# Kernel optimization log

Hardware: AMD Instinct MI355X
Metric: run time of the kernel (lower is better)

The kernel has to match this reference:

```python
import jax, jax.numpy as jnp
import numpy as np

# SamplesLoss(loss='sinkhorn', p=1, blur=0.05): entropic regularization eps = blur**p = 0.05,
# debiased Sinkhorn divergence S(a,b) = OT(a,b) - 0.5*OT(a,a) - 0.5*OT(b,b).
EPS = 0.05
N_ITER = 50
N_POINTS = 32


def _cost(X, Y):
    # p=1 cost: Euclidean distance. X:[B,N,D] Y:[B,M,D] -> [B,N,M]
    d2 = jnp.sum((X[:, :, None, :] - Y[:, None, :, :]) ** 2, axis=-1)
    return jnp.sqrt(d2 + 1e-12)


def _ot(X, Y):
    # log-domain Sinkhorn with uniform weights; returns dual cost <mu,f>+<nu,g> per batch.
    B, N, _ = X.shape
    M = Y.shape[1]
    C = _cost(X, Y)  # [B,N,M]
    log_mu = jnp.full((B, N), -np.log(N), C.dtype)
    log_nu = jnp.full((B, M), -np.log(M), C.dtype)

    def body(carry, _):
        f, g = carry
        f = -EPS * jax.nn.logsumexp((g[:, None, :] - C) / EPS + log_nu[:, None, :], axis=2)
        g = -EPS * jax.nn.logsumexp((f[:, :, None] - C) / EPS + log_mu[:, :, None], axis=1)
        return (f, g), None

    init = (jnp.zeros((B, N), C.dtype), jnp.zeros((B, M), C.dtype))
    (f, g), _ = jax.lax.scan(body, init, None, length=N_ITER)
    return jnp.mean(f, axis=-1) + jnp.mean(g, axis=-1)  # uniform weights => mean


def _sinkhorn_div(X, Y):
    return _ot(X, Y) - 0.5 * _ot(X, X) - 0.5 * _ot(Y, Y)


def _encode(x, W, edge_index):
    # simple 1-layer GCN-style encoder: linear + mean neighbor aggregation + self, ReLU
    h = x @ W  # [n_nodes, emb_dim]
    src, dst = edge_index[0], edge_index[1]
    n = x.shape[0]
    agg = jax.ops.segment_sum(h[src], dst, num_segments=n)
    deg = jax.ops.segment_sum(jnp.ones(src.shape, h.dtype), dst, num_segments=n)
    return jax.nn.relu(h + agg / jnp.maximum(deg, 1.0)[:, None])


def setup_inputs() -> dict:
    key = jax.random.key(0)
    k1, k2, k3, k4, k5 = jax.random.split(key, 5)
    n_nodes, d_feat, emb_dim = 50000, 128, 256
    n_edges, n_pairs = 800000, 8192
    x = jax.random.normal(k1, (n_nodes, d_feat), jnp.float32)
    W = jax.random.normal(k2, (d_feat, emb_dim), jnp.float32) / np.sqrt(d_feat)
    edge_index = jax.random.randint(k3, (2, n_edges), 0, n_nodes, jnp.int64)
    pairs = jax.random.randint(k4, (2, n_pairs), 0, n_nodes, jnp.int64)
    graph_dist = jax.random.uniform(k5, (n_pairs,), jnp.float32, 1.0, 5.0)
    return {"x": x, "W": W, "edge_index": edge_index, "pairs": pairs,
            "graph_dist": graph_dist}


def reference(x, W, edge_index, pairs, graph_dist):
    z = _encode(x, W, edge_index)                       # [n_nodes, emb_dim]
    B = pairs.shape[1]
    Xa = z[pairs[0]].reshape(B, N_POINTS, -1)           # [B, n_points, space_dim]
    Xb = z[pairs[1]].reshape(B, N_POINTS, -1)
    distance = _sinkhorn_div(Xa, Xb)                    # = -score_pairs
    distortion = jnp.abs(distance - graph_dist) / graph_dist
    return jnp.mean(distortion)
```

## Files before the change

kernel.cpp:

```cpp
#include <hip/hip_runtime.h>

#define N_NODES 50000
#define N_EDGES 800000
#define N_PAIRS 8192
#define N_SLOTS (2 * N_PAIRS)
#define CAP     64

#define INV_EPS   20.0f
#define LOG2E_F   1.4426950408889634f
#define LN2_F     0.6931471805599453f
#define LN32_F    3.4657359027997265f
#define EPS_F     0.05f

typedef float f2 __attribute__((ext_vector_type(2)));

__global__ void k_mark(const int* __restrict__ pairs, int* __restrict__ flags) {
    int t = blockIdx.x * 256 + threadIdx.x;
    if (t < N_SLOTS) flags[pairs[t]] = 1;
}

__global__ __launch_bounds__(256) void k_scatter(
        const int* __restrict__ eidx, const int* __restrict__ flags,
        int* __restrict__ cnt, int* __restrict__ bucket) {
    int t = blockIdx.x * 256 + threadIdx.x;
    int dst = eidx[N_EDGES + t];
    if (!flags[dst]) return;
    int pos = atomicAdd(&cnt[dst], 1);
    if (pos < CAP) bucket[dst * CAP + pos] = eidx[t];
}

__global__ __launch_bounds__(256) void k_gemm(
        const int* __restrict__ pairs, const float* __restrict__ x,
        const int* __restrict__ cnt, const int* __restrict__ bucket,
        const float* __restrict__ W, float* __restrict__ Z) {
    __shared__ __align__(16) float Us[16 * 128];
    int sbase = blockIdx.x * 16;
    int t = threadIdx.x;
    int wave = t >> 6, lane = t & 63;

    #pragma unroll
    for (int rr = 0; rr < 4; ++rr) {
        int r = wave * 4 + rr;
        int node = pairs[sbase + r];
        int n = cnt[node];
        int m = (n < CAP) ? n : CAP;
        const int* bk = bucket + node * CAP;
        float ax = 0.0f, ay = 0.0f;
        int k = 0;
        for (; k + 4 <= m; k += 4) {
            int s0 = bk[k], s1 = bk[k + 1], s2 = bk[k + 2], s3 = bk[k + 3];
            float2 v0 = *(const float2*)(x + (size_t)s0 * 128 + lane * 2);
            float2 v1 = *(const float2*)(x + (size_t)s1 * 128 + lane * 2);
            float2 v2 = *(const float2*)(x + (size_t)s2 * 128 + lane * 2);
            float2 v3 = *(const float2*)(x + (size_t)s3 * 128 + lane * 2);
            ax += (v0.x + v1.x) + (v2.x + v3.x);
            ay += (v0.y + v1.y) + (v2.y + v3.y);
        }
        for (; k < m; ++k) {
            int s0 = bk[k];
            float2 v0 = *(const float2*)(x + (size_t)s0 * 128 + lane * 2);
            ax += v0.x;
            ay += v0.y;
        }
        float rdeg = 1.0f / fmaxf((float)n, 1.0f);
        float2 xv = *(const float2*)(x + (size_t)node * 128 + lane * 2);
        float2 o;
        o.x = fmaf(ax, rdeg, xv.x);
        o.y = fmaf(ay, rdeg, xv.y);
        *(float2*)(Us + r * 128 + lane * 2) = o;
    }
    __syncthreads();

    int jq = t & 63;
    int rq = t >> 6;
    float acc[4][4] = {};
    const float4* Wv = (const float4*)W;

    for (int k4 = 0; k4 < 32; ++k4) {
        float4 wv[4];
        #pragma unroll
        for (int i = 0; i < 4; ++i) wv[i] = Wv[(size_t)(k4 * 4 + i) * 64 + jq];
        #pragma unroll
        for (int r = 0; r < 4; ++r) {
            float4 uv = *(const float4*)(Us + (rq * 4 + r) * 128 + k4 * 4);
            float uk0 = uv.x, uk1 = uv.y, uk2 = uv.z, uk3 = uv.w;
            acc[r][0] = fmaf(uk0, wv[0].x, acc[r][0]);
            acc[r][1] = fmaf(uk0, wv[0].y, acc[r][1]);
            acc[r][2] = fmaf(uk0, wv[0].z, acc[r][2]);
            acc[r][3] = fmaf(uk0, wv[0].w, acc[r][3]);
            acc[r][0] = fmaf(uk1, wv[1].x, acc[r][0]);
            acc[r][1] = fmaf(uk1, wv[1].y, acc[r][1]);
            acc[r][2] = fmaf(uk1, wv[1].z, acc[r][2]);
            acc[r][3] = fmaf(uk1, wv[1].w, acc[r][3]);
            acc[r][0] = fmaf(uk2, wv[2].x, acc[r][0]);
            acc[r][1] = fmaf(uk2, wv[2].y, acc[r][1]);
            acc[r][2] = fmaf(uk2, wv[2].z, acc[r][2]);
            acc[r][3] = fmaf(uk2, wv[2].w, acc[r][3]);
            acc[r][0] = fmaf(uk3, wv[3].x, acc[r][0]);
            acc[r][1] = fmaf(uk3, wv[3].y, acc[r][1]);
            acc[r][2] = fmaf(uk3, wv[3].z, acc[r][2]);
            acc[r][3] = fmaf(uk3, wv[3].w, acc[r][3]);
        }
    }

    #pragma unroll
    for (int r = 0; r < 4; ++r) {
        float4 o;
        o.x = fmaxf(acc[r][0], 0.0f);
        o.y = fmaxf(acc[r][1], 0.0f);
        o.z = fmaxf(acc[r][2], 0.0f);
        o.w = fmaxf(acc[r][3], 0.0f);
        *(float4*)(Z + (size_t)(sbase + rq * 4 + r) * 256 + jq * 4) = o;
    }
}

__global__ __launch_bounds__(128) void k_sinkhorn(
        const float* __restrict__ Z, float* __restrict__ dist) {
    __shared__ __align__(16) float smem[2][640];

    int w = threadIdx.x >> 6;
    int lane = threadIdx.x & 63;
    const float CSCALE = -INV_EPS * LOG2E_F;
    const float CBIAS  = -LN32_F * LOG2E_F;

    if (blockIdx.x >= 4096) {
        float* sX = &smem[w][0];
        float* sY = &smem[w][256];
        float* sf = &smem[w][512];
        float* sg = &smem[w][544];
        float* su = &smem[w][576];
        float* sv = &smem[w][608];

        int b = (blockIdx.x - 4096) * 2 + w;
        int sx = b, sy = N_PAIRS + b;

        *(float4*)(&sX[lane * 4]) = ((const float4*)(Z + (size_t)sx * 256))[lane];
        *(float4*)(&sY[lane * 4]) = ((const float4*)(Z + (size_t)sy * 256))[lane];
        sg[lane & 31] = 0.0f;

        int i_r = lane & 31, jh = lane >> 5;
        int j_c = lane & 31, ih = lane >> 5;

        f2 CrowV[8], CcolV[8];
        {
            const f2* xp = (const f2*)(&sX[i_r * 8]);
            f2 x0 = xp[0], x1 = xp[1], x2 = xp[2], x3 = xp[3];
            #pragma unroll
            for (int t = 0; t < 16; ++t) {
                int j = jh * 16 + t;
                const f2* yp = (const f2*)(&sY[j * 8]);
                f2 d, s2;
                d = x0 - yp[0]; s2 = d * d;
                d = x1 - yp[1]; s2 = __builtin_elementwise_fma(d, d, s2);
                d = x2 - yp[2]; s2 = __builtin_elementwise_fma(d, d, s2);
                d = x3 - yp[3]; s2 = __builtin_elementwise_fma(d, d, s2);
                float d2 = s2.x + s2.y + 1e-12f;
                CrowV[t >> 1][t & 1] = fmaf(__builtin_amdgcn_sqrtf(d2), CSCALE, CBIAS);
            }
            const f2* yp = (const f2*)(&sY[j_c * 8]);
            f2 y0 = yp[0], y1 = yp[1], y2 = yp[2], y3 = yp[3];
            #pragma unroll
            for (int t = 0; t < 16; ++t) {
                int i = ih * 16 + t;
                const f2* qp = (const f2*)(&sX[i * 8]);
                f2 d, s2;
                d = qp[0] - y0; s2 = d * d;
                d = qp[1] - y1; s2 = __builtin_elementwise_fma(d, d, s2);
                d = qp[2] - y2; s2 = __builtin_elementwise_fma(d, d, s2);
                d = qp[3] - y3; s2 = __builtin_elementwise_fma(d, d, s2);
                float d2 = s2.x + s2.y + 1e-12f;
                CcolV[t >> 1][t & 1] = fmaf(__builtin_amdgcn_sqrtf(d2), CSCALE, CBIAS);
            }
        }

        float ft = 0.0f, gt = 0.0f;

        #pragma unroll 1
        for (int it = 0; it < 2; ++it) {
            {
                const float4* gp = (const float4*)(&sg[jh * 16]);
                float4 G0 = gp[0], G1 = gp[1], G2 = gp[2], G3 = gp[3];
                f2 gv[8] = {f2{G0.x, G0.y}, f2{G0.z, G0.w}, f2{G1.x, G1.y}, f2{G1.z, G1.w},
                            f2{G2.x, G2.y}, f2{G2.z, G2.w}, f2{G3.x, G3.y}, f2{G3.z, G3.w}};
                f2 val[8], m2 = f2{-1e30f, -1e30f};
                #pragma unroll
                for (int t2 = 0; t2 < 8; ++t2) {
                    val[t2] = gv[t2] + CrowV[t2];
                    m2 = __builtin_elementwise_max(m2, val[t2]);
                }
                float m = fmaxf(m2.x, m2.y);
                m = fmaxf(m, __shfl_xor(m, 32));
                f2 mm = f2{m, m};
                float s0 = 0.0f, s1 = 0.0f;
                #pragma unroll
                for (int t2 = 0; t2 < 8; ++t2) {
                    f2 e = val[t2] - mm;
                    s0 += __builtin_amdgcn_exp2f(e.x);
                    s1 += __builtin_amdgcn_exp2f(e.y);
                }
                float s = s0 + s1;
                s += __shfl_xor(s, 32);
                ft = -(m + __builtin_amdgcn_logf(s));
            }
            sf[lane & 31] = ft;
            {
                const float4* fp = (const float4*)(&sf[ih * 16]);
                float4 F0 = fp[0], F1 = fp[1], F2 = fp[2], F3 = fp[3];
                f2 fv[8] = {f2{F0.x, F0.y}, f2{F0.z, F0.w}, f2{F1.x, F1.y}, f2{F1.z, F1.w},
                            f2{F2.x, F2.y}, f2{F2.z, F2.w}, f2{F3.x, F3.y}, f2{F3.z, F3.w}};
                f2 val[8], m2 = f2{-1e30f, -1e30f};
                #pragma unroll
                for (int t2 = 0; t2 < 8; ++t2) {
                    val[t2] = fv[t2] + CcolV[t2];
                    m2 = __builtin_elementwise_max(m2, val[t2]);
                }
                float m = fmaxf(m2.x, m2.y);
                m = fmaxf(m, __shfl_xor(m, 32));
                f2 mm = f2{m, m};
                float s0 = 0.0f, s1 = 0.0f;
                #pragma unroll
                for (int t2 = 0; t2 < 8; ++t2) {
                    f2 e = val[t2] - mm;
                    s0 += __builtin_amdgcn_exp2f(e.x);
                    s1 += __builtin_amdgcn_exp2f(e.y);
                }
                float s = s0 + s1;
                s += __shfl_xor(s, 32);
                gt = -(m + __builtin_amdgcn_logf(s));
            }
            sg[lane & 31] = gt;
        }

        f2 KR2[8], KC2[8];
        float ureg = 1.0f, vreg = 1.0f;

        auto absorb = [&]() {
            const float4* gp = (const float4*)(&sg[jh * 16]);
            float4 G0 = gp[0], G1 = gp[1], G2 = gp[2], G3 = gp[3];
            f2 gv[8] = {f2{G0.x, G0.y}, f2{G0.z, G0.w}, f2{G1.x, G1.y}, f2{G1.z, G1.w},
                        f2{G2.x, G2.y}, f2{G2.z, G2.w}, f2{G3.x, G3.y}, f2{G3.z, G3.w}};
            f2 ftv = f2{ft, ft};
            #pragma unroll
            for (int t2 = 0; t2 < 8; ++t2) {
                f2 a = (gv[t2] + CrowV[t2]) + ftv;
                KR2[t2].x = __builtin_amdgcn_exp2f(a.x);
                KR2[t2].y = __builtin_amdgcn_exp2f(a.y);
            }
            const float4* fp = (const float4*)(&sf[ih * 16]);
            float4 F0 = fp[0], F1 = fp[1], F2 = fp[2], F3 = fp[3];
            f2 fv[8] = {f2{F0.x, F0.y}, f2{F0.z, F0.w}, f2{F1.x, F1.y}, f2{F1.z, F1.w},
                        f2{F2.x, F2.y}, f2{F2.z, F2.w}, f2{F3.x, F3.y}, f2{F3.z, F3.w}};
            f2 gtv = f2{gt, gt};
            #pragma unroll
            for (int t2 = 0; t2 < 8; ++t2) {
                f2 a = (fv[t2] + CcolV[t2]) + gtv;
                KC2[t2].x = __builtin_amdgcn_exp2f(a.x);
                KC2[t2].y = __builtin_amdgcn_exp2f(a.y);
            }
            sv[lane & 31] = 1.0f;
            ureg = 1.0f;
            vreg = 1.0f;
        };

        const int blens[5] = {6, 6, 12, 12, 12};
        absorb();
        #pragma unroll 1
        for (int blk = 0; blk < 5; ++blk) {
            int L = blens[blk];
            #pragma unroll 2
            for (int s6 = 0; s6 < L; ++s6) {
                {
                    const float4* vp = (const float4*)(&sv[jh * 16]);
                    float4 A0 = vp[0], A1 = vp[1], A2 = vp[2], A3 = vp[3];
                    f2 acc0 = KR2[0] * f2{A0.x, A0.y};
                    f2 acc1 = KR2[1] * f2{A0.z, A0.w};
                    acc0 = __builtin_elementwise_fma(KR2[2], f2{A1.x, A1.y}, acc0);
                    acc1 = __builtin_elementwise_fma(KR2[3], f2{A1.z, A1.w}, acc1);
                    acc0 = __builtin_elementwise_fma(KR2[4], f2{A2.x, A2.y}, acc0);
                    acc1 = __builtin_elementwise_fma(KR2[5], f2{A2.z, A2.w}, acc1);
                    acc0 = __builtin_elementwise_fma(KR2[6], f2{A3.x, A3.y}, acc0);
                    acc1 = __builtin_elementwise_fma(KR2[7], f2{A3.z, A3.w}, acc1);
                    f2 a = acc0 + acc1;
                    float S = a.x + a.y;
                    S += __shfl_xor(S, 32);
                    ureg = __builtin_amdgcn_rcpf(S);
                }
                su[lane & 31] = ureg;
                {
                    const float4* up = (const float4*)(&su[ih * 16]);
                    float4 A0 = up[0], A1 = up[1], A2 = up[2], A3 = up[3];
                    f2 acc0 = KC2[0] * f2{A0.x, A0.y};
                    f2 acc1 = KC2[1] * f2{A0.z, A0.w};
                    acc0 = __builtin_elementwise_fma(KC2[2], f2{A1.x, A1.y}, acc0);
                    acc1 = __builtin_elementwise_fma(KC2[3], f2{A1.z, A1.w}, acc1);
                    acc0 = __builtin_elementwise_fma(KC2[4], f2{A2.x, A2.y}, acc0);
                    acc1 = __builtin_elementwise_fma(KC2[5], f2{A2.z, A2.w}, acc1);
                    acc0 = __builtin_elementwise_fma(KC2[6], f2{A3.x, A3.y}, acc0);
                    acc1 = __builtin_elementwise_fma(KC2[7], f2{A3.z, A3.w}, acc1);
                    f2 a = acc0 + acc1;
                    float T = a.x + a.y;
                    T += __shfl_xor(T, 32);
                    vreg = __builtin_amdgcn_rcpf(T);
                }
                sv[lane & 31] = vreg;
            }
            if (blk < 4) {
                ft += __builtin_amdgcn_logf(ureg);
                gt += __builtin_amdgcn_logf(vreg);
                sf[lane & 31] = ft;
                sg[lane & 31] = gt;
                absorb();
            }
        }
        ft += __builtin_amdgcn_logf(ureg);
        gt += __builtin_amdgcn_logf(vreg);

        float v = ft + gt;
        #pragma unroll
        for (int off = 32; off > 0; off >>= 1) v += __shfl_xor(v, off);
        if (lane == 0) {
            float cost = v * (EPS_F * LN2_F / 64.0f);
            unsafeAtomicAdd(&dist[b], cost);
        }
    } else {
        int h = lane >> 5, i = lane & 31;
        int q = (i >> 4) & 1;
        int ip = i ^ 16;
        int P = blockIdx.x * 2 + w;
        int src = h ? (N_PAIRS + P) : P;

        float* sP  = &smem[w][h * 256];
        float* swv = &smem[w][512];
        float* spv = &smem[w][576];

        {
            const float4* zp = (const float4*)(Z + (size_t)src * 256);
            *(float4*)(&sP[i * 8])     = zp[i * 2];
            *(float4*)(&sP[i * 8 + 4]) = zp[i * 2 + 1];
        }

        f2 CA[8], CB[8];
        {
            const f2* xp = (const f2*)(&sP[i * 8]);
            f2 x0 = xp[0], x1 = xp[1], x2 = xp[2], x3 = xp[3];
            const f2* bp = (const f2*)(&sP[ip * 8]);
            f2 b0 = bp[0], b1 = bp[1], b2 = bp[2], b3 = bp[3];
            #pragma unroll
            for (int t = 0; t < 16; ++t) {
                int j = q * 16 + t;
                const f2* yp = (const f2*)(&sP[j * 8]);
                f2 y0 = yp[0], y1 = yp[1], y2 = yp[2], y3 = yp[3];
                f2 d, s2;
                d = x0 - y0; s2 = d * d;
                d = x1 - y1; s2 = __builtin_elementwise_fma(d, d, s2);
                d = x2 - y2; s2 = __builtin_elementwise_fma(d, d, s2);
                d = x3 - y3; s2 = __builtin_elementwise_fma(d, d, s2);
                float d2 = s2.x + s2.y + 1e-12f;
                CA[t >> 1][t & 1] = fmaf(__builtin_amdgcn_sqrtf(d2), CSCALE, CBIAS);
                d = b0 - y0; s2 = d * d;
                d = b1 - y1; s2 = __builtin_elementwise_fma(d, d, s2);
                d = b2 - y2; s2 = __builtin_elementwise_fma(d, d, s2);
                d = b3 - y3; s2 = __builtin_elementwise_fma(d, d, s2);
                float e2 = s2.x + s2.y + 1e-12f;
                CB[t >> 1][t & 1] = fmaf(__builtin_amdgcn_sqrtf(e2), CSCALE, CBIAS);
            }
        }

        float pp = 0.0f, E = 1.0f, wcur = 1.0f, wprev = 1.0f;
        f2 KA[8], KB[8];
        #pragma unroll
        for (int t = 0; t < 8; ++t) {
            KA[t].x = __builtin_amdgcn_exp2f(CA[t].x);
            KA[t].y = __builtin_amdgcn_exp2f(CA[t].y);
            KB[t].x = __builtin_amdgcn_exp2f(CB[t].x);
            KB[t].y = __builtin_amdgcn_exp2f(CB[t].y);
        }
        swv[lane] = 1.0f;

        const int blens[9] = {4, 12, 12, 12, 12, 12, 12, 12, 12};
        #pragma unroll 1
        for (int blk = 0; blk < 9; ++blk) {
            int L = blens[blk];
            #pragma unroll 2
            for (int s = 0; s < L; ++s) {
                const float4* wp = (const float4*)(&swv[h * 32 + q * 16]);
                float4 A0 = wp[0], A1 = wp[1], A2 = wp[2], A3 = wp[3];
                f2 aA0 = KA[0] * f2{A0.x, A0.y};
                f2 aA1 = KA[1] * f2{A0.z, A0.w};
                f2 aB0 = KB[0] * f2{A0.x, A0.y};
                f2 aB1 = KB[1] * f2{A0.z, A0.w};
                aA0 = __builtin_elementwise_fma(KA[2], f2{A1.x, A1.y}, aA0);
                aA1 = __builtin_elementwise_fma(KA[3], f2{A1.z, A1.w}, aA1);
                aB0 = __builtin_elementwise_fma(KB[2], f2{A1.x, A1.y}, aB0);
                aB1 = __builtin_elementwise_fma(KB[3], f2{A1.z, A1.w}, aB1);
                aA0 = __builtin_elementwise_fma(KA[4], f2{A2.x, A2.y}, aA0);
                aA1 = __builtin_elementwise_fma(KA[5], f2{A2.z, A2.w}, aA1);
                aB0 = __builtin_elementwise_fma(KB[4], f2{A2.x, A2.y}, aB0);
                aB1 = __builtin_elementwise_fma(KB[5], f2{A2.z, A2.w}, aB1);
                aA0 = __builtin_elementwise_fma(KA[6], f2{A3.x, A3.y}, aA0);
                aA1 = __builtin_elementwise_fma(KA[7], f2{A3.z, A3.w}, aA1);
                aB0 = __builtin_elementwise_fma(KB[6], f2{A3.x, A3.y}, aB0);
                aB1 = __builtin_elementwise_fma(KB[7], f2{A3.z, A3.w}, aB1);
                f2 aa = aA0 + aA1;
                f2 bb = aB0 + aB1;
                float pa = aa.x + aa.y;
                float pb = bb.x + bb.y;
                float other = __shfl_xor(pb, 16);
                float S = pa + other;
                wprev = wcur;
                wcur = __builtin_amdgcn_rcpf(S) * E;
                swv[h * 32 + i] = wcur;
            }
            if (blk < 8) {
                pp += __builtin_amdgcn_logf(wcur);
                spv[lane] = pp;
                const float4* pv = (const float4*)(&spv[h * 32 + q * 16]);
                float4 P0 = pv[0], P1 = pv[1], P2 = pv[2], P3 = pv[3];
                f2 pj[8] = {f2{P0.x,P0.y}, f2{P0.z,P0.w}, f2{P1.x,P1.y}, f2{P1.z,P1.w},
                            f2{P2.x,P2.y}, f2{P2.z,P2.w}, f2{P3.x,P3.y}, f2{P3.z,P3.w}};
                #pragma unroll
                for (int t = 0; t < 8; ++t) {
                    f2 a = pj[t] + CA[t];
                    KA[t].x = __builtin_amdgcn_exp2f(a.x);
                    KA[t].y = __builtin_amdgcn_exp2f(a.y);
                    f2 c = pj[t] + CB[t];
                    KB[t].x = __builtin_amdgcn_exp2f(c.x);
                    KB[t].y = __builtin_amdgcn_exp2f(c.y);
                }
                E = __builtin_amdgcn_exp2f(-pp);
                wcur = 1.0f;
                swv[lane] = 1.0f;
            }
        }

        float zsum = 2.0f * pp + __builtin_amdgcn_logf(wprev)
                   + __builtin_amdgcn_logf(wcur);
        #pragma unroll
        for (int off = 16; off > 0; off >>= 1) zsum += __shfl_xor(zsum, off);
        if (i == 0) {
            float cost = zsum * (EPS_F * LN2_F / 32.0f);
            unsafeAtomicAdd(&dist[P], -0.5f * cost);
        }
    }
}

__global__ void k_finalize(const float* __restrict__ dist,
                           const float* __restrict__ gd, float* __restrict__ out) {
    __shared__ float red[256];
    float s = 0.0f;
    for (int i = threadIdx.x; i < N_PAIRS; i += 256) {
        float g = gd[i];
        s += fabsf(dist[i] - g) / g;
    }
    red[threadIdx.x] = s;
    __syncthreads();
    for (int o = 128; o > 0; o >>= 1) {
        if (threadIdx.x < o) red[threadIdx.x] += red[threadIdx.x + o];
        __syncthreads();
    }
    if (threadIdx.x == 0) out[0] = red[0] * (1.0f / N_PAIRS);
}

extern "C" void kernel_launch(void* const* d_in, const int* in_sizes, int n_in,
                              void* d_out, int out_size, void* d_ws, size_t ws_size,
                              hipStream_t stream) {
    const float* x    = (const float*)d_in[0];
    const float* W    = (const float*)d_in[1];
    const int*   eidx = (const int*)d_in[2];
    const int*   pair = (const int*)d_in[3];
    const float* gd   = (const float*)d_in[4];

    char* ws = (char*)d_ws;
    size_t off = 0;
    int*   cnt    = (int*)  (ws + off); off += (size_t)N_NODES * 4;
    int*   flags  = (int*)  (ws + off); off += (size_t)N_NODES * 4;
    float* dist   = (float*)(ws + off); off += (size_t)N_PAIRS * 4;
    size_t zero_bytes = off;
    int*   bucket = (int*)  (ws + off); off += (size_t)N_NODES * CAP * 4;
    float* Z      = (float*)(ws + off); off += (size_t)N_SLOTS * 256 * 4;

    hipMemsetAsync(d_ws, 0, zero_bytes, stream);
    k_mark    <<<(N_SLOTS + 255) / 256, 256, 0, stream>>>(pair, flags);
    k_scatter <<<N_EDGES / 256, 256, 0, stream>>>(eidx, flags, cnt, bucket);
    k_gemm    <<<N_SLOTS / 16, 256, 0, stream>>>(pair, x, cnt, bucket, W, Z);
    k_sinkhorn<<<8192, 128, 0, stream>>>(Z, dist);
    k_finalize<<<1, 256, 0, stream>>>(dist, gd, (float*)d_out);
}
```

Baseline: 252.0 us.

## Process one cross-pair per half-wave and update Sinkhorn kernels multiplicatively

The cross OT(X,Y) path now gives each 32-lane half-wave a whole problem, one row per lane, instead of splitting rows across two halves that needed cross-half shuffles. This halves the blocks needed for the cross pairs, so the launch shrinks from 8192 to 6144 blocks. Both paths now refresh the Gibbs kernel at each absorption by multiplying the existing entries by exp of the dual increments, rather than recomputing exp from the full potentials. Registers per lane roughly double (32-entry cost rows and columns), which may lower occupancy, and the multiplicative update may accumulate rounding drift.

```diff
diff --git a/kernel.cpp b/kernel.cpp
--- a/kernel.cpp
+++ b/kernel.cpp
@@ -116,222 +116,24 @@
 
 __global__ __launch_bounds__(128) void k_sinkhorn(
         const float* __restrict__ Z, float* __restrict__ dist) {
-    __shared__ __align__(16) float smem[2][640];
+    __shared__ __align__(16) float smem[2][1280];
 
     int w = threadIdx.x >> 6;
     int lane = threadIdx.x & 63;
+    float* S = &smem[w][0];
     const float CSCALE = -INV_EPS * LOG2E_F;
     const float CBIAS  = -LN32_F * LOG2E_F;
 
-    if (blockIdx.x >= 4096) {
-        float* sX = &smem[w][0];
-        float* sY = &smem[w][256];
-        float* sf = &smem[w][512];
-        float* sg = &smem[w][544];
-        float* su = &smem[w][576];
-        float* sv = &smem[w][608];
-
-        int b = (blockIdx.x - 4096) * 2 + w;
-        int sx = b, sy = N_PAIRS + b;
-
-        *(float4*)(&sX[lane * 4]) = ((const float4*)(Z + (size_t)sx * 256))[lane];
-        *(float4*)(&sY[lane * 4]) = ((const float4*)(Z + (size_t)sy * 256))[lane];
-        sg[lane & 31] = 0.0f;
-
-        int i_r = lane & 31, jh = lane >> 5;
-        int j_c = lane & 31, ih = lane >> 5;
-
-        f2 CrowV[8], CcolV[8];
-        {
-            const f2* xp = (const f2*)(&sX[i_r * 8]);
-            f2 x0 = xp[0], x1 = xp[1], x2 = xp[2], x3 = xp[3];
-            #pragma unroll
-            for (int t = 0; t < 16; ++t) {
-                int j = jh * 16 + t;
-                const f2* yp = (const f2*)(&sY[j * 8]);
-                f2 d, s2;
-                d = x0 - yp[0]; s2 = d * d;
-                d = x1 - yp[1]; s2 = __builtin_elementwise_fma(d, d, s2);
-                d = x2 - yp[2]; s2 = __builtin_elementwise_fma(d, d, s2);
-                d = x3 - yp[3]; s2 = __builtin_elementwise_fma(d, d, s2);
-                float d2 = s2.x + s2.y + 1e-12f;
-                CrowV[t >> 1][t & 1] = fmaf(__builtin_amdgcn_sqrtf(d2), CSCALE, CBIAS);
-            }
-            const f2* yp = (const f2*)(&sY[j_c * 8]);
-            f2 y0 = yp[0], y1 = yp[1], y2 = yp[2], y3 = yp[3];
-            #pragma unroll
-            for (int t = 0; t < 16; ++t) {
-                int i = ih * 16 + t;
-                const f2* qp = (const f2*)(&sX[i * 8]);
-                f2 d, s2;
-                d = qp[0] - y0; s2 = d * d;
-                d = qp[1] - y1; s2 = __builtin_elementwise_fma(d, d, s2);
-                d = qp[2] - y2; s2 = __builtin_elementwise_fma(d, d, s2);
-                d = qp[3] - y3; s2 = __builtin_elementwise_fma(d, d, s2);
-                float d2 = s2.x + s2.y + 1e-12f;
-                CcolV[t >> 1][t & 1] = fmaf(__builtin_amdgcn_sqrtf(d2), CSCALE, CBIAS);
-            }
-        }
-
-        float ft = 0.0f, gt = 0.0f;
-
-        #pragma unroll 1
-        for (int it = 0; it < 2; ++it) {
-            {
-                const float4* gp = (const float4*)(&sg[jh * 16]);
-                float4 G0 = gp[0], G1 = gp[1], G2 = gp[2], G3 = gp[3];
-                f2 gv[8] = {f2{G0.x, G0.y}, f2{G0.z, G0.w}, f2{G1.x, G1.y}, f2{G1.z, G1.w},
-                            f2{G2.x, G2.y}, f2{G2.z, G2.w}, f2{G3.x, G3.y}, f2{G3.z, G3.w}};
-                f2 val[8], m2 = f2{-1e30f, -1e30f};
-                #pragma unroll
-                for (int t2 = 0; t2 < 8; ++t2) {
-                    val[t2] = gv[t2] + CrowV[t2];
-                    m2 = __builtin_elementwise_max(m2, val[t2]);
-                }
-                float m = fmaxf(m2.x, m2.y);
-                m = fmaxf(m, __shfl_xor(m, 32));
-                f2 mm = f2{m, m};
-                float s0 = 0.0f, s1 = 0.0f;
-                #pragma unroll
-                for (int t2 = 0; t2 < 8; ++t2) {
-                    f2 e = val[t2] - mm;
-                    s0 += __builtin_amdgcn_exp2f(e.x);
-                    s1 += __builtin_amdgcn_exp2f(e.y);
-                }
-                float s = s0 + s1;
-                s += __shfl_xor(s, 32);
-                ft = -(m + __builtin_amdgcn_logf(s));
-            }
-            sf[lane & 31] = ft;
-            {
-                const float4* fp = (const float4*)(&sf[ih * 16]);
-                float4 F0 = fp[0], F1 = fp[1], F2 = fp[2], F3 = fp[3];
-                f2 fv[8] = {f2{F0.x, F0.y}, f2{F0.z, F0.w}, f2{F1.x, F1.y}, f2{F1.z, F1.w},
-                            f2{F2.x, F2.y}, f2{F2.z, F2.w}, f2{F3.x, F3.y}, f2{F3.z, F3.w}};
-                f2 val[8], m2 = f2{-1e30f, -1e30f};
-                #pragma unroll
-                for (int t2 = 0; t2 < 8; ++t2) {
-                    val[t2] = fv[t2] + CcolV[t2];
-                    m2 = __builtin_elementwise_max(m2, val[t2]);
-                }
-                float m = fmaxf(m2.x, m2.y);
-                m = fmaxf(m, __shfl_xor(m, 32));
-                f2 mm = f2{m, m};
-                float s0 = 0.0f, s1 = 0.0f;
-                #pragma unroll
-                for (int t2 = 0; t2 < 8; ++t2) {
-                    f2 e = val[t2] - mm;
-                    s0 += __builtin_amdgcn_exp2f(e.x);
-                    s1 += __builtin_amdgcn_exp2f(e.y);
-                }
-                float s = s0 + s1;
-                s += __shfl_xor(s, 32);
-                gt = -(m + __builtin_amdgcn_logf(s));
-            }
-            sg[lane & 31] = gt;
-        }
-
-        f2 KR2[8], KC2[8];
-        float ureg = 1.0f, vreg = 1.0f;
-
-        auto absorb = [&]() {
-            const float4* gp = (const float4*)(&sg[jh * 16]);
-            float4 G0 = gp[0], G1 = gp[1], G2 = gp[2], G3 = gp[3];
-            f2 gv[8] = {f2{G0.x, G0.y}, f2{G0.z, G0.w}, f2{G1.x, G1.y}, f2{G1.z, G1.w},
-                        f2{G2.x, G2.y}, f2{G2.z, G2.w}, f2{G3.x, G3.y}, f2{G3.z, G3.w}};
-            f2 ftv = f2{ft, ft};
-            #pragma unroll
-            for (int t2 = 0; t2 < 8; ++t2) {
-                f2 a = (gv[t2] + CrowV[t2]) + ftv;
-                KR2[t2].x = __builtin_amdgcn_exp2f(a.x);
-                KR2[t2].y = __builtin_amdgcn_exp2f(a.y);
-            }
-            const float4* fp = (const float4*)(&sf[ih * 16]);
-            float4 F0 = fp[0], F1 = fp[1], F2 = fp[2], F3 = fp[3];
-            f2 fv[8] = {f2{F0.x, F0.y}, f2{F0.z, F0.w}, f2{F1.x, F1.y}, f2{F1.z, F1.w},
-                        f2{F2.x, F2.y}, f2{F2.z, F2.w}, f2{F3.x, F3.y}, f2{F3.z, F3.w}};
-            f2 gtv = f2{gt, gt};
-            #pragma unroll
-            for (int t2 = 0; t2 < 8; ++t2) {
-                f2 a = (fv[t2] + CcolV[t2]) + gtv;
-                KC2[t2].x = __builtin_amdgcn_exp2f(a.x);
-                KC2[t2].y = __builtin_amdgcn_exp2f(a.y);
-            }
-            sv[lane & 31] = 1.0f;
-            ureg = 1.0f;
-            vreg = 1.0f;
-        };
-
-        const int blens[5] = {6, 6, 12, 12, 12};
-        absorb();
-        #pragma unroll 1
-        for (int blk = 0; blk < 5; ++blk) {
-            int L = blens[blk];
-            #pragma unroll 2
-            for (int s6 = 0; s6 < L; ++s6) {
-                {
-                    const float4* vp = (const float4*)(&sv[jh * 16]);
-                    float4 A0 = vp[0], A1 = vp[1], A2 = vp[2], A3 = vp[3];
-                    f2 acc0 = KR2[0] * f2{A0.x, A0.y};
-                    f2 acc1 = KR2[1] * f2{A0.z, A0.w};
-                    acc0 = __builtin_elementwise_fma(KR2[2], f2{A1.x, A1.y}, acc0);
-                    acc1 = __builtin_elementwise_fma(KR2[3], f2{A1.z, A1.w}, acc1);
-                    acc0 = __builtin_elementwise_fma(KR2[4], f2{A2.x, A2.y}, acc0);
-                    acc1 = __builtin_elementwise_fma(KR2[5], f2{A2.z, A2.w}, acc1);
-                    acc0 = __builtin_elementwise_fma(KR2[6], f2{A3.x, A3.y}, acc0);
-                    acc1 = __builtin_elementwise_fma(KR2[7], f2{A3.z, A3.w}, acc1);
-                    f2 a = acc0 + acc1;
-                    float S = a.x + a.y;
-                    S += __shfl_xor(S, 32);
-                    ureg = __builtin_amdgcn_rcpf(S);
-                }
-                su[lane & 31] = ureg;
-                {
-                    const float4* up = (const float4*)(&su[ih * 16]);
-                    float4 A0 = up[0], A1 = up[1], A2 = up[2], A3 = up[3];
-                    f2 acc0 = KC2[0] * f2{A0.x, A0.y};
-                    f2 acc1 = KC2[1] * f2{A0.z, A0.w};
-                    acc0 = __builtin_elementwise_fma(KC2[2], f2{A1.x, A1.y}, acc0);
-                    acc1 = __builtin_elementwise_fma(KC2[3], f2{A1.z, A1.w}, acc1);
-                    acc0 = __builtin_elementwise_fma(KC2[4], f2{A2.x, A2.y}, acc0);
-                    acc1 = __builtin_elementwise_fma(KC2[5], f2{A2.z, A2.w}, acc1);
-                    acc0 = __builtin_elementwise_fma(KC2[6], f2{A3.x, A3.y}, acc0);
-                    acc1 = __builtin_elementwise_fma(KC2[7], f2{A3.z, A3.w}, acc1);
-                    f2 a = acc0 + acc1;
-                    float T = a.x + a.y;
-                    T += __shfl_xor(T, 32);
-                    vreg = __builtin_amdgcn_rcpf(T);
-                }
-                sv[lane & 31] = vreg;
-            }
-            if (blk < 4) {
-                ft += __builtin_amdgcn_logf(ureg);
-                gt += __builtin_amdgcn_logf(vreg);
-                sf[lane & 31] = ft;
-                sg[lane & 31] = gt;
-                absorb();
-            }
-        }
-        ft += __builtin_amdgcn_logf(ureg);
-        gt += __builtin_amdgcn_logf(vreg);
-
-        float v = ft + gt;
-        #pragma unroll
-        for (int off = 32; off > 0; off >>= 1) v += __shfl_xor(v, off);
-        if (lane == 0) {
-            float cost = v * (EPS_F * LN2_F / 64.0f);
-            unsafeAtomicAdd(&dist[b], cost);
-        }
-    } else {
+    if (blockIdx.x < 4096) {
         int h = lane >> 5, i = lane & 31;
         int q = (i >> 4) & 1;
         int ip = i ^ 16;
         int P = blockIdx.x * 2 + w;
         int src = h ? (N_PAIRS + P) : P;
 
-        float* sP  = &smem[w][h * 256];
-        float* swv = &smem[w][512];
-        float* spv = &smem[w][576];
+        float* sP  = S + h * 256;
+        float* swv = S + 512;
+        float* spv = S + 576;
 
         {
             const float4* zp = (const float4*)(Z + (size_t)src * 256);
@@ -406,26 +208,39 @@
                 float pa = aa.x + aa.y;
                 float pb = bb.x + bb.y;
                 float other = __shfl_xor(pb, 16);
-                float S = pa + other;
+                float Sv = pa + other;
                 wprev = wcur;
-                wcur = __builtin_amdgcn_rcpf(S) * E;
+                wcur = __builtin_amdgcn_rcpf(Sv) * E;
                 swv[h * 32 + i] = wcur;
             }
             if (blk < 8) {
-                pp += __builtin_amdgcn_logf(wcur);
-                spv[lane] = pp;
-                const float4* pv = (const float4*)(&spv[h * 32 + q * 16]);
-                float4 P0 = pv[0], P1 = pv[1], P2 = pv[2], P3 = pv[3];
-                f2 pj[8] = {f2{P0.x,P0.y}, f2{P0.z,P0.w}, f2{P1.x,P1.y}, f2{P1.z,P1.w},
-                            f2{P2.x,P2.y}, f2{P2.z,P2.w}, f2{P3.x,P3.y}, f2{P3.z,P3.w}};
-                #pragma unroll
-                for (int t = 0; t < 8; ++t) {
-                    f2 a = pj[t] + CA[t];
-                    KA[t].x = __builtin_amdgcn_exp2f(a.x);
-                    KA[t].y = __builtin_amdgcn_exp2f(a.y);
-                    f2 c = pj[t] + CB[t];
-                    KB[t].x = __builtin_amdgcn_exp2f(c.x);
-                    KB[t].y = __builtin_amdgcn_exp2f(c.y);
+                float d = __builtin_amdgcn_logf(wcur);
+                pp += d;
+                spv[h * 32 + i] = d;
+                const float4* dv = (const float4*)(&spv[h * 32 + q * 16]);
+                float4 D0 = dv[0], D1 = dv[1], D2 = dv[2], D3 = dv[3];
+                float ex[16];
+                ex[0]  = __builtin_amdgcn_exp2f(D0.x);
+                ex[1]  = __builtin_amdgcn_exp2f(D0.y);
+                ex[2]  = __builtin_amdgcn_exp2f(D0.z);
+                ex[3]  = __builtin_amdgcn_exp2f(D0.w);
+                ex[4]  = __builtin_amdgcn_exp2f(D1.x);
+                ex[5]  = __builtin_amdgcn_exp2f(D1.y);
+                ex[6]  = __builtin_amdgcn_exp2f(D1.z);
+                ex[7]  = __builtin_amdgcn_exp2f(D1.w);
+                ex[8]  = __builtin_amdgcn_exp2f(D2.x);
+                ex[9]  = __builtin_amdgcn_exp2f(D2.y);
+                ex[10] = __builtin_amdgcn_exp2f(D2.z);
+                ex[11] = __builtin_amdgcn_exp2f(D2.w);
+                ex[12] = __builtin_amdgcn_exp2f(D3.x);
+                ex[13] = __builtin_amdgcn_exp2f(D3.y);
+                ex[14] = __builtin_amdgcn_exp2f(D3.z);
+                ex[15] = __builtin_amdgcn_exp2f(D3.w);
+                #pragma unroll
+                for (int t2 = 0; t2 < 8; ++t2) {
+                    f2 ee = f2{ex[2 * t2], ex[2 * t2 + 1]};
+                    KA[t2] *= ee;
+                    KB[t2] *= ee;
                 }
                 E = __builtin_amdgcn_exp2f(-pp);
                 wcur = 1.0f;
@@ -440,6 +255,223 @@
         if (i == 0) {
             float cost = zsum * (EPS_F * LN2_F / 32.0f);
             unsafeAtomicAdd(&dist[P], -0.5f * cost);
+        }
+    } else {
+        int h = lane >> 5, l = lane & 31;
+        int p = (blockIdx.x - 4096) * 4 + w * 2 + h;
+
+        float* base = S + h * 640;
+        float* sX = base;
+        float* sY = base + 256;
+        float* sf = base + 512;
+        float* sg = base + 544;
+        float* su = base + 576;
+        float* sv = base + 608;
+
+        {
+            const float4* zx = (const float4*)(Z + (size_t)p * 256);
+            const float4* zy = (const float4*)(Z + (size_t)(N_PAIRS + p) * 256);
+            *(float4*)(&sX[l * 8])     = zx[l * 2];
+            *(float4*)(&sX[l * 8 + 4]) = zx[l * 2 + 1];
+            *(float4*)(&sY[l * 8])     = zy[l * 2];
+            *(float4*)(&sY[l * 8 + 4]) = zy[l * 2 + 1];
+        }
+        sg[l] = 0.0f;
+
+        f2 Crow[16], Ccol[16];
+        {
+            const f2* xp = (const f2*)(&sX[l * 8]);
+            f2 x0 = xp[0], x1 = xp[1], x2 = xp[2], x3 = xp[3];
+            const f2* yp = (const f2*)(&sY[l * 8]);
+            f2 y0 = yp[0], y1 = yp[1], y2 = yp[2], y3 = yp[3];
+            #pragma unroll
+            for (int t = 0; t < 32; ++t) {
+                const f2* op = (const f2*)(&sY[t * 8]);
+                f2 d, s2;
+                d = x0 - op[0]; s2 = d * d;
+                d = x1 - op[1]; s2 = __builtin_elementwise_fma(d, d, s2);
+                d = x2 - op[2]; s2 = __builtin_elementwise_fma(d, d, s2);
+                d = x3 - op[3]; s2 = __builtin_elementwise_fma(d, d, s2);
+                float d2 = s2.x + s2.y + 1e-12f;
+                Crow[t >> 1][t & 1] = fmaf(__builtin_amdgcn_sqrtf(d2), CSCALE, CBIAS);
+                const f2* qp = (const f2*)(&sX[t * 8]);
+                d = qp[0] - y0; s2 = d * d;
+                d = qp[1] - y1; s2 = __builtin_elementwise_fma(d, d, s2);
+                d = qp[2] - y2; s2 = __builtin_elementwise_fma(d, d, s2);
+                d = qp[3] - y3; s2 = __builtin_elementwise_fma(d, d, s2);
+                float e2 = s2.x + s2.y + 1e-12f;
+                Ccol[t >> 1][t & 1] = fmaf(__builtin_amdgcn_sqrtf(e2), CSCALE, CBIAS);
+            }
+        }
+
+        float ft = 0.0f, gt = 0.0f;
+
+        #pragma unroll 1
+        for (int it = 0; it < 2; ++it) {
+            {
+                const float4* gp = (const float4*)sg;
+                float4 G[8];
+                #pragma unroll
+                for (int r = 0; r < 8; ++r) G[r] = gp[r];
+                f2 val[16], m2 = f2{-1e30f, -1e30f};
+                #pragma unroll
+                for (int r = 0; r < 8; ++r) {
+                    val[2 * r]     = f2{G[r].x, G[r].y} + Crow[2 * r];
+                    val[2 * r + 1] = f2{G[r].z, G[r].w} + Crow[2 * r + 1];
+                    m2 = __builtin_elementwise_max(m2, val[2 * r]);
+                    m2 = __builtin_elementwise_max(m2, val[2 * r + 1]);
+                }
+                float m = fmaxf(m2.x, m2.y);
+                f2 mm = f2{m, m};
+                float s0 = 0.0f, s1 = 0.0f;
+                #pragma unroll
+                for (int t2 = 0; t2 < 16; ++t2) {
+                    f2 e = val[t2] - mm;
+                    s0 += __builtin_amdgcn_exp2f(e.x);
+                    s1 += __builtin_amdgcn_exp2f(e.y);
+                }
+                ft = -(m + __builtin_amdgcn_logf(s0 + s1));
+            }
+            sf[l] = ft;
+            {
+                const float4* fp = (const float4*)sf;
+                float4 F[8];
+                #pragma unroll
+                for (int r = 0; r < 8; ++r) F[r] = fp[r];
+                f2 val[16], m2 = f2{-1e30f, -1e30f};
+                #pragma unroll
+                for (int r = 0; r < 8; ++r) {
+                    val[2 * r]     = f2{F[r].x, F[r].y} + Ccol[2 * r];
+                    val[2 * r + 1] = f2{F[r].z, F[r].w} + Ccol[2 * r + 1];
+                    m2 = __builtin_elementwise_max(m2, val[2 * r]);
+                    m2 = __builtin_elementwise_max(m2, val[2 * r + 1]);
+                }
+                float m = fmaxf(m2.x, m2.y);
+                f2 mm = f2{m, m};
+                float s0 = 0.0f, s1 = 0.0f;
+                #pragma unroll
+                for (int t2 = 0; t2 < 16; ++t2) {
+                    f2 e = val[t2] - mm;
+                    s0 += __builtin_amdgcn_exp2f(e.x);
+                    s1 += __builtin_amdgcn_exp2f(e.y);
+                }
+                gt = -(m + __builtin_amdgcn_logf(s0 + s1));
+            }
+            sg[l] = gt;
+        }
+
+        f2 KR[16], KC[16];
+        {
+            const float4* gp = (const float4*)sg;
+            #pragma unroll
+            for (int r = 0; r < 8; ++r) {
+                float4 G = gp[r];
+                f2 a0 = f2{G.x, G.y} + Crow[2 * r] + f2{ft, ft};
+                f2 a1 = f2{G.z, G.w} + Crow[2 * r + 1] + f2{ft, ft};
+                KR[2 * r].x     = __builtin_amdgcn_exp2f(a0.x);
+                KR[2 * r].y     = __builtin_amdgcn_exp2f(a0.y);
+                KR[2 * r + 1].x = __builtin_amdgcn_exp2f(a1.x);
+                KR[2 * r + 1].y = __builtin_amdgcn_exp2f(a1.y);
+            }
+            const float4* fp = (const float4*)sf;
+            #pragma unroll
+            for (int r = 0; r < 8; ++r) {
+                float4 F = fp[r];
+                f2 a0 = f2{F.x, F.y} + Ccol[2 * r] + f2{gt, gt};
+                f2 a1 = f2{F.z, F.w} + Ccol[2 * r + 1] + f2{gt, gt};
+                KC[2 * r].x     = __builtin_amdgcn_exp2f(a0.x);
+                KC[2 * r].y     = __builtin_amdgcn_exp2f(a0.y);
+                KC[2 * r + 1].x = __builtin_amdgcn_exp2f(a1.x);
+                KC[2 * r + 1].y = __builtin_amdgcn_exp2f(a1.y);
+            }
+        }
+        sv[l] = 1.0f;
+        float ureg = 1.0f, vreg = 1.0f;
+
+        const int blens[5] = {6, 6, 12, 12, 12};
+        #pragma unroll 1
+        for (int blk = 0; blk < 5; ++blk) {
+            int L = blens[blk];
+            #pragma unroll 2
+            for (int s6 = 0; s6 < L; ++s6) {
+                {
+                    const float4* vp = (const float4*)sv;
+                    f2 acc0, acc1;
+                    float4 A = vp[0];
+                    acc0 = KR[0] * f2{A.x, A.y};
+                    acc1 = KR[1] * f2{A.z, A.w};
+                    #pragma unroll
+                    for (int r = 1; r < 8; ++r) {
+                        float4 B = vp[r];
+                        acc0 = __builtin_elementwise_fma(KR[2 * r],     f2{B.x, B.y}, acc0);
+                        acc1 = __builtin_elementwise_fma(KR[2 * r + 1], f2{B.z, B.w}, acc1);
+                    }
+                    f2 a = acc0 + acc1;
+                    ureg = __builtin_amdgcn_rcpf(a.x + a.y);
+                }
+                su[l] = ureg;
+                {
+                    const float4* up = (const float4*)su;
+                    f2 acc0, acc1;
+                    float4 A = up[0];
+                    acc0 = KC[0] * f2{A.x, A.y};
+                    acc1 = KC[1] * f2{A.z, A.w};
+                    #pragma unroll
+                    for (int r = 1; r < 8; ++r) {
+                        float4 B = up[r];
+                        acc0 = __builtin_elementwise_fma(KC[2 * r],     f2{B.x, B.y}, acc0);
+                        acc1 = __builtin_elementwise_fma(KC[2 * r + 1], f2{B.z, B.w}, acc1);
+                    }
+                    f2 a = acc0 + acc1;
+                    vreg = __builtin_amdgcn_rcpf(a.x + a.y);
+                }
+                sv[l] = vreg;
+            }
+            if (blk < 4) {
+                float df = __builtin_amdgcn_logf(ureg);
+                float dg = __builtin_amdgcn_logf(vreg);
+                ft += df;
+                gt += dg;
+                sf[l] = df;
+                sg[l] = dg;
+                const float4* dgv = (const float4*)sg;
+                #pragma unroll
+                for (int r = 0; r < 8; ++r) {
+                    float4 D = dgv[r];
+                    f2 e0, e1;
+                    e0.x = __builtin_amdgcn_exp2f(df + D.x);
+                    e0.y = __builtin_amdgcn_exp2f(df + D.y);
+                    e1.x = __builtin_amdgcn_exp2f(df + D.z);
+                    e1.y = __builtin_amdgcn_exp2f(df + D.w);
+                    KR[2 * r]     *= e0;
+                    KR[2 * r + 1] *= e1;
+                }
+                const float4* dfv = (const float4*)sf;
+                #pragma unroll
+                for (int r = 0; r < 8; ++r) {
+                    float4 D = dfv[r];
+                    f2 e0, e1;
+                    e0.x = __builtin_amdgcn_exp2f(dg + D.x);
+                    e0.y = __builtin_amdgcn_exp2f(dg + D.y);
+                    e1.x = __builtin_amdgcn_exp2f(dg + D.z);
+                    e1.y = __builtin_amdgcn_exp2f(dg + D.w);
+                    KC[2 * r]     *= e0;
+                    KC[2 * r + 1] *= e1;
+                }
+                sv[l] = 1.0f;
+                ureg = 1.0f;
+                vreg = 1.0f;
+            }
+        }
+        ft += __builtin_amdgcn_logf(ureg);
+        gt += __builtin_amdgcn_logf(vreg);
+
+        float v = ft + gt;
+        #pragma unroll
+        for (int off = 16; off > 0; off >>= 1) v += __shfl_xor(v, off);
+        if (l == 0) {
+            float cost = v * (EPS_F * LN2_F / 32.0f);
+            unsafeAtomicAdd(&dist[p], cost);
         }
     }
 }
@@ -483,6 +515,6 @@
     k_mark    <<<(N_SLOTS + 255) / 256, 256, 0, stream>>>(pair, flags);
     k_scatter <<<N_EDGES / 256, 256, 0, stream>>>(eidx, flags, cnt, bucket);
     k_gemm    <<<N_SLOTS / 16, 256, 0, stream>>>(pair, x, cnt, bucket, W, Z);
-    k_sinkhorn<<<8192, 128, 0, stream>>>(Z, dist);
+    k_sinkhorn<<<6144, 128, 0, stream>>>(Z, dist);
     k_finalize<<<1, 256, 0, stream>>>(dist, gd, (float*)d_out);
 }
```

Measured after the change: 246.2 us, median of 2. 2.3% less time.
